# Optimization experiments

Hardware: AMD Instinct MI355X
Metric: run time of the kernel (lower is better)

## Reference

```python
import jax, jax.numpy as jnp
import numpy as np

SIGMA = 1.0


def setup_inputs() -> dict:
    key = jax.random.key(0)
    k1, k2, k3 = jax.random.split(key, 3)
    N, M, D = 4096, 8192, 512
    x = jax.random.normal(k1, (N, D), dtype=jnp.float32)
    patterns = jax.random.normal(k2, (M, D), dtype=jnp.float32)
    targets = jax.random.randint(k3, (M,), 0, 2, dtype=jnp.int64)
    return {"x": x, "patterns": patterns, "targets": targets}


def reference(x, patterns, targets):
    # pairwise squared Euclidean distances via the expansion trick (GEMM-dominated)
    x2 = jnp.sum(x * x, axis=1, keepdims=True)            # [N, 1]
    p2 = jnp.sum(patterns * patterns, axis=1)             # [M]
    cross = x @ patterns.T                                # [N, M]
    sq_dist = jnp.maximum(x2 + p2[None, :] - 2.0 * cross, 0.0)
    kernel = jnp.exp(-sq_dist / (2.0 * SIGMA ** 2))       # [N, M]

    normal_mask = (targets == 0).astype(kernel.dtype)     # [M]
    anomaly_mask = (targets == 1).astype(kernel.dtype)
    n_normal = jnp.maximum(jnp.sum(normal_mask), 1.0)
    n_anomaly = jnp.maximum(jnp.sum(anomaly_mask), 1.0)
    normal_output = (kernel @ normal_mask) / n_normal     # [N]
    anomaly_output = (kernel @ anomaly_mask) / n_anomaly  # [N]
    return jnp.stack([normal_output, anomaly_output], axis=1)  # [N, 2]
```

## Files before the change

### kernel.cpp

```cpp
#include <hip/hip_runtime.h>
#include <hip/hip_bf16.h>
#include <stdint.h>

#define N_X 4096
#define M_P 8192
#define D_K 512

#define BM 256
#define BN 256
#define BK 32
#define NKT (D_K / BK)

typedef __attribute__((ext_vector_type(8))) short bf16x8;
typedef __attribute__((ext_vector_type(4))) float f32x4;

__device__ __forceinline__ unsigned short f2bf(float f) {
    union { float f; unsigned u; } c; c.f = f;
    unsigned u = c.u;
    return (unsigned short)((u + 0x7FFFu + ((u >> 16) & 1u)) >> 16);
}

__device__ __forceinline__ void gload_lds16(const void* g, void* l) {
    __builtin_amdgcn_global_load_lds(
        (const __attribute__((address_space(1))) void*)g,
        (__attribute__((address_space(3))) void*)l,
        16, 0, 0);
}

__global__ void prep_rows(const float* __restrict__ x,
                          const float* __restrict__ pat,
                          unsigned short* __restrict__ xb,
                          unsigned short* __restrict__ pb,
                          float* __restrict__ x2, float* __restrict__ p2) {
    int gw   = (int)((blockIdx.x * blockDim.x + threadIdx.x) >> 6);
    int lane = (int)(threadIdx.x & 63);
    const float* src; unsigned short* dst; float* nrm; int row;
    if (gw < N_X) { src = x;   dst = xb; nrm = x2; row = gw; }
    else          { src = pat; dst = pb; nrm = p2; row = gw - N_X; }
    const float* r = src + (size_t)row * D_K;
    float4 v0 = *(const float4*)(r + lane * 4);
    float4 v1 = *(const float4*)(r + 256 + lane * 4);
    float s = v0.x * v0.x + v0.y * v0.y + v0.z * v0.z + v0.w * v0.w
            + v1.x * v1.x + v1.y * v1.y + v1.z * v1.z + v1.w * v1.w;
    ushort4 p0, p1;
    p0.x = f2bf(v0.x); p0.y = f2bf(v0.y); p0.z = f2bf(v0.z); p0.w = f2bf(v0.w);
    p1.x = f2bf(v1.x); p1.y = f2bf(v1.y); p1.z = f2bf(v1.z); p1.w = f2bf(v1.w);
    unsigned short* d = dst + (size_t)row * D_K;
    *(ushort4*)(d + lane * 4)       = p0;
    *(ushort4*)(d + 256 + lane * 4) = p1;
#pragma unroll
    for (int m = 32; m; m >>= 1) s += __shfl_xor(s, m);
    if (lane == 0) nrm[row] = s;
}

__global__ void count_targets(const int* __restrict__ t, float* __restrict__ inv) {
    __shared__ int part[4];
    int c = 0;
    for (int m = (int)threadIdx.x; m < M_P / 4; m += 256) {
        int4 v = ((const int4*)t)[m];
        c += v.x + v.y + v.z + v.w;
    }
#pragma unroll
    for (int m = 32; m; m >>= 1) c += __shfl_xor(c, m);
    if ((threadIdx.x & 63) == 0) part[threadIdx.x >> 6] = c;
    __syncthreads();
    if (threadIdx.x == 0) {
        int n1 = part[0] + part[1] + part[2] + part[3];
        int n0 = M_P - n1;
        inv[0] = 1.0f / fmaxf((float)n0, 1.0f);
        inv[1] = 1.0f / fmaxf((float)n1, 1.0f);
    }
}

__global__ __launch_bounds__(512, 2) void pnn_main(
    const unsigned short* __restrict__ xb, const unsigned short* __restrict__ pb,
    const float* __restrict__ x2, const float* __restrict__ p2,
    const int* __restrict__ tgt, const float* __restrict__ invc,
    float* __restrict__ out) {
    __shared__ unsigned short As[2][BM][BK];
    __shared__ unsigned short Bs[2][BN][BK];

    const int tid  = (int)threadIdx.x;
    const int wid  = tid >> 6;
    const int lane = tid & 63;
    const int wr   = wid >> 2;
    const int wc   = wid & 3;
    const int lr   = lane & 15;
    const int lg   = lane >> 4;

    const int wg  = (int)blockIdx.x;
    const int xcd = wg & 7, idx = wg >> 3;
    const int mr = xcd & 1, nr = xcd >> 1;
    const int tileM = (mr * 8 + (idx & 7)) * BM;
    const int tileN = (nr * 8 + (idx >> 3)) * BN;

    f32x4 acc[8][4];
#pragma unroll
    for (int i = 0; i < 8; ++i)
#pragma unroll
        for (int j = 0; j < 4; ++j)
            acc[i][j] = (f32x4){0.f, 0.f, 0.f, 0.f};

    auto stage = [&](int buf, int k0) {
        const int rsub = wid * 16 + (lane >> 2);
        const int col  = (lane & 3) * 8;
#pragma unroll
        for (int i = 0; i < 2; ++i) {
            gload_lds16(xb + (size_t)(tileM + i * 128 + rsub) * D_K + k0 + col,
                        &As[buf][i * 128 + wid * 16][0]);
            gload_lds16(pb + (size_t)(tileN + i * 128 + rsub) * D_K + k0 + col,
                        &Bs[buf][i * 128 + wid * 16][0]);
        }
    };

    stage(0, 0);
    asm volatile("s_waitcnt vmcnt(0)" ::: "memory");
    __builtin_amdgcn_s_barrier();

    for (int kt = 0; kt < NKT; ++kt) {
        const int cur = kt & 1;
        if (kt + 1 < NKT) stage(cur ^ 1, (kt + 1) * BK);

        bf16x8 a[8], b[4];
#pragma unroll
        for (int mi = 0; mi < 8; ++mi)
            a[mi] = *(const bf16x8*)&As[cur][wr * 128 + mi * 16 + lr][lg * 8];
#pragma unroll
        for (int nj = 0; nj < 4; ++nj)
            b[nj] = *(const bf16x8*)&Bs[cur][wc * 64 + nj * 16 + lr][lg * 8];

        __builtin_amdgcn_s_setprio(1);
#pragma unroll
        for (int mi = 0; mi < 8; ++mi)
#pragma unroll
            for (int nj = 0; nj < 4; ++nj)
                acc[mi][nj] = __builtin_amdgcn_mfma_f32_16x16x32_bf16(
                    a[mi], b[nj], acc[mi][nj], 0, 0, 0);
        __builtin_amdgcn_s_setprio(0);

        if (kt + 1 < NKT) {
            asm volatile("s_waitcnt lgkmcnt(0)" ::: "memory");
            asm volatile("s_waitcnt vmcnt(0)" ::: "memory");
            __builtin_amdgcn_s_barrier();
        }
    }

    const float inv0 = invc[0], inv1 = invc[1];
    float p2c[4], w1[4];
#pragma unroll
    for (int nj = 0; nj < 4; ++nj) {
        int m = tileN + wc * 64 + nj * 16 + lr;
        p2c[nj] = p2[m];
        w1[nj] = (float)tgt[m];
    }
#pragma unroll
    for (int mi = 0; mi < 8; ++mi) {
#pragma unroll
        for (int r = 0; r < 4; ++r) {
            int n = tileM + wr * 128 + mi * 16 + lg * 4 + r;
            float xn = x2[n];
            float s0 = 0.f, s1 = 0.f;
#pragma unroll
            for (int nj = 0; nj < 4; ++nj) {
                float c = acc[mi][nj][r];
                float d = fmaxf(xn + p2c[nj] - 2.0f * c, 0.0f);
                float k = __expf(-0.5f * d);
                float k1 = k * w1[nj];
                s1 += k1;
                s0 += k - k1;
            }
#pragma unroll
            for (int msk = 1; msk < 16; msk <<= 1) {
                s0 += __shfl_xor(s0, msk);
                s1 += __shfl_xor(s1, msk);
            }
            if (lr == 0) {
                atomicAdd(&out[2 * n + 0], s0 * inv0);
                atomicAdd(&out[2 * n + 1], s1 * inv1);
            }
        }
    }
}

extern "C" void kernel_launch(void* const* d_in, const int* in_sizes, int n_in,
                              void* d_out, int out_size, void* d_ws, size_t ws_size,
                              hipStream_t stream) {
    const float* x   = (const float*)d_in[0];
    const float* pat = (const float*)d_in[1];
    const int*   tgt = (const int*)d_in[2];
    float* out = (float*)d_out;

    char* w = (char*)d_ws;
    unsigned short* xb = (unsigned short*)w;
    unsigned short* pb = (unsigned short*)(w + (size_t)N_X * D_K * 2);
    float* x2   = (float*)(w + (size_t)(N_X + M_P) * D_K * 2);
    float* p2   = x2 + N_X;
    float* invc = p2 + M_P;

    hipMemsetAsync(d_out, 0, sizeof(float) * 2 * N_X, stream);
    prep_rows<<<(N_X + M_P) / 4, 256, 0, stream>>>(x, pat, xb, pb, x2, p2);
    count_targets<<<1, 256, 0, stream>>>(tgt, invc);
    pnn_main<<<(N_X / BM) * (M_P / BN), 512, 0, stream>>>(
        xb, pb, x2, p2, tgt, invc, out);
}
```

Baseline: 178.3 us.

## Triple-buffer LDS tiles with prefetch distance two and XOR-swizzle LDS layout

Moves the GEMM main loop from double to triple buffering, so global-to-LDS loads for tile k+2 are issued while tile k is computed. It replaces the full vmcnt(0) drain with partial vmcnt waits. It also XOR-swizzles the 16-byte column chunks, both when staging into LDS and when reading fragments, to reduce LDS bank conflicts on the 64-byte-stride rows. The trade-off is that LDS per block grows to 96KB, which may no longer allow two blocks per CU as the launch bounds intend.

```diff
diff --git a/kernel.cpp b/kernel.cpp
--- a/kernel.cpp
+++ b/kernel.cpp
@@ -77,8 +77,8 @@
     const float* __restrict__ x2, const float* __restrict__ p2,
     const int* __restrict__ tgt, const float* __restrict__ invc,
     float* __restrict__ out) {
-    __shared__ unsigned short As[2][BM][BK];
-    __shared__ unsigned short Bs[2][BN][BK];
+    __shared__ unsigned short As[3][BM][BK];
+    __shared__ unsigned short Bs[3][BN][BK];
 
     const int tid  = (int)threadIdx.x;
     const int wid  = tid >> 6;
@@ -101,33 +101,40 @@
         for (int j = 0; j < 4; ++j)
             acc[i][j] = (f32x4){0.f, 0.f, 0.f, 0.f};
 
-    auto stage = [&](int buf, int k0) {
-        const int rsub = wid * 16 + (lane >> 2);
-        const int col  = (lane & 3) * 8;
+    auto stage = [&](int b, int k0) {
+        const int r  = wid * 16 + (lane >> 2);
+        const int ce = (((lane & 3) ^ ((lane >> 3) & 3)) * 8);
 #pragma unroll
         for (int i = 0; i < 2; ++i) {
-            gload_lds16(xb + (size_t)(tileM + i * 128 + rsub) * D_K + k0 + col,
-                        &As[buf][i * 128 + wid * 16][0]);
-            gload_lds16(pb + (size_t)(tileN + i * 128 + rsub) * D_K + k0 + col,
-                        &Bs[buf][i * 128 + wid * 16][0]);
+            gload_lds16(xb + (size_t)(tileM + i * 128 + r) * D_K + k0 + ce,
+                        &As[b][i * 128 + wid * 16][0]);
+            gload_lds16(pb + (size_t)(tileN + i * 128 + r) * D_K + k0 + ce,
+                        &Bs[b][i * 128 + wid * 16][0]);
         }
     };
 
-    stage(0, 0);
-    asm volatile("s_waitcnt vmcnt(0)" ::: "memory");
-    __builtin_amdgcn_s_barrier();
-
+    stage(0, 0 * BK);
+    stage(1, 1 * BK);
+
+    const int asw = (lg ^ ((lr >> 1) & 3)) * 8;
+
+#pragma unroll
     for (int kt = 0; kt < NKT; ++kt) {
-        const int cur = kt & 1;
-        if (kt + 1 < NKT) stage(cur ^ 1, (kt + 1) * BK);
-
-        bf16x8 a[8], b[4];
+        const int b = kt % 3;
+        if (kt + 2 < NKT) stage((kt + 2) % 3, (kt + 2) * BK);
+
+        if (kt + 2 < NKT)      asm volatile("s_waitcnt vmcnt(8)" ::: "memory");
+        else if (kt + 1 < NKT) asm volatile("s_waitcnt vmcnt(4)" ::: "memory");
+        else                   asm volatile("s_waitcnt vmcnt(0)" ::: "memory");
+        __builtin_amdgcn_s_barrier();
+
+        bf16x8 a[8], bfr[4];
 #pragma unroll
         for (int mi = 0; mi < 8; ++mi)
-            a[mi] = *(const bf16x8*)&As[cur][wr * 128 + mi * 16 + lr][lg * 8];
+            a[mi] = *(const bf16x8*)&As[b][wr * 128 + mi * 16 + lr][asw];
 #pragma unroll
         for (int nj = 0; nj < 4; ++nj)
-            b[nj] = *(const bf16x8*)&Bs[cur][wc * 64 + nj * 16 + lr][lg * 8];
+            bfr[nj] = *(const bf16x8*)&Bs[b][wc * 64 + nj * 16 + lr][asw];
 
         __builtin_amdgcn_s_setprio(1);
 #pragma unroll
@@ -135,12 +142,11 @@
 #pragma unroll
             for (int nj = 0; nj < 4; ++nj)
                 acc[mi][nj] = __builtin_amdgcn_mfma_f32_16x16x32_bf16(
-                    a[mi], b[nj], acc[mi][nj], 0, 0, 0);
+                    a[mi], bfr[nj], acc[mi][nj], 0, 0, 0);
         __builtin_amdgcn_s_setprio(0);
 
-        if (kt + 1 < NKT) {
+        if (kt + 3 < NKT) {
             asm volatile("s_waitcnt lgkmcnt(0)" ::: "memory");
-            asm volatile("s_waitcnt vmcnt(0)" ::: "memory");
             __builtin_amdgcn_s_barrier();
         }
     }
```

After: 176.2 us. No clear change (-1.2%).
